# Optimization experiments

Hardware: AMD Instinct MI355X
Metric: run time of the kernel (lower is better)

The kernel has to match this reference:

```python
import jax, jax.numpy as jnp
import numpy as np

C_M, C_Z, NO_BINS = 256, 128, 15
MIN_BIN, MAX_BIN, INF = 3.25, 20.75, 1e8
LN_EPS = 1e-5


def _layer_norm(t, w, b):
    mu = jnp.mean(t, axis=-1, keepdims=True)
    var = jnp.var(t, axis=-1, keepdims=True)
    return (t - mu) * jax.lax.rsqrt(var + LN_EPS) * w + b


def setup_inputs() -> dict:
    key = jax.random.key(0)
    ks = jax.random.split(key, 8)
    B, N = 1, 768
    m = jax.random.normal(ks[0], (B, N, C_M), dtype=jnp.float32)
    z = jax.random.normal(ks[1], (B, N, N, C_Z), dtype=jnp.float32)
    # scale coords so pairwise distances span the 3.25-20.75 A bin range
    x = jax.random.normal(ks[2], (B, N, 3), dtype=jnp.float32) * 10.0
    seqs = jax.random.normal(ks[3], (B, N, 21), dtype=jnp.float32)
    lin_w = jax.random.normal(ks[4], (C_Z, NO_BINS), dtype=jnp.float32) * 0.1
    lin_b = jnp.zeros((C_Z,), dtype=jnp.float32)
    ln_m_w = jnp.ones((C_M,), dtype=jnp.float32)
    ln_m_b = jnp.zeros((C_M,), dtype=jnp.float32)
    ln_z_w = jnp.ones((C_Z,), dtype=jnp.float32)
    ln_z_b = jnp.zeros((C_Z,), dtype=jnp.float32)
    return {"m": m, "z": z, "x": x, "seqs": seqs,
            "lin_w": lin_w, "lin_b": lin_b,
            "ln_m_w": ln_m_w, "ln_m_b": ln_m_b,
            "ln_z_w": ln_z_w, "ln_z_b": ln_z_b}


def reference(m, z, x, seqs, lin_w, lin_b, ln_m_w, ln_m_b, ln_z_w, ln_z_b):
    # m update: LayerNorm only (track_seq_states=False, seqs unused)
    m_update = _layer_norm(m, ln_m_w, ln_m_b)

    bins = jnp.linspace(MIN_BIN, MAX_BIN, NO_BINS, dtype=x.dtype)
    sq_bins = bins ** 2
    upper = jnp.concatenate([sq_bins[1:], jnp.array([INF], dtype=x.dtype)])

    # pairwise squared distances [*, N, N, 1]
    diff = x[..., :, None, :] - x[..., None, :, :]
    d = jnp.sum(diff ** 2, axis=-1, keepdims=True)
    # one-hot distogram [*, N, N, no_bins] (strict inequalities, matching torch)
    oh = ((d > sq_bins) & (d < upper)).astype(x.dtype)
    # Linear(no_bins -> c_z)
    d_emb = jnp.einsum('...b,cb->...c', oh, lin_w) + lin_b

    z_update = d_emb + _layer_norm(z, ln_z_w, ln_z_b)
    return (m_update, z_update)
```

## Files before the change

kernel.cpp:

```cpp
#include <hip/hip_runtime.h>

#define LN_EPS 1e-5f
#define C_M 256
#define C_Z 128
#define NO_BINS 15

typedef float f4 __attribute__((ext_vector_type(4)));

__device__ __forceinline__ f4 f4zero() { f4 t = {0.f, 0.f, 0.f, 0.f}; return t; }

__device__ __forceinline__ int bin_of_xj(const float* __restrict__ x,
                                         const float* sqb, int i,
                                         float xj0, float xj1, float xj2)
{
    const float dx = x[3 * i + 0] - xj0;
    const float dy = x[3 * i + 1] - xj1;
    const float dz = x[3 * i + 2] - xj2;
    const float d = __fadd_rn(__fadd_rn(__fmul_rn(dx, dx), __fmul_rn(dy, dy)),
                              __fmul_rn(dz, dz));
    int cnt = 0;
#pragma unroll
    for (int k = 0; k < NO_BINS; ++k) {
        const float bk = 3.25f + 1.25f * (float)k;
        cnt += (d > bk * bk) ? 1 : 0;
    }
    return ((cnt > 0) && (d < 1e8f) && (d != sqb[cnt])) ? cnt - 1 : -1;
}

__device__ __forceinline__ void ln_stats(const f4 v, float& s, float& s2)
{
    s  = v.x + v.y + v.z + v.w;
    s2 = v.x * v.x + v.y * v.y + v.z * v.z + v.w * v.w;
}

__global__ __launch_bounds__(256, 6) void fused_uniform(
    const float* __restrict__ m, const float* __restrict__ ln_m_w,
    const float* __restrict__ ln_m_b, float* __restrict__ out_m, int m_rows,
    const float* __restrict__ z, const float* __restrict__ x,
    const float* __restrict__ lin_w, const float* __restrict__ lin_b,
    const float* __restrict__ ln_z_w, const float* __restrict__ ln_z_b,
    float* __restrict__ out_z, int N, int iters)
{
    __shared__ float lw[NO_BINS * C_Z];
    __shared__ float sqb[16];
    const int tid = threadIdx.x;
    for (int t = tid; t < NO_BINS * C_Z; t += 256) {
        const int c = t / NO_BINS;
        const int bin = t - c * NO_BINS;
        lw[bin * C_Z + c] = lin_w[t];
    }
    if (tid < 16) {
        const float bk = 3.25f + 1.25f * (float)tid;
        sqb[tid] = (tid < NO_BINS) ? bk * bk : -1.0f;
    }
    __syncthreads();

    if ((int)blockIdx.x < ((m_rows + 3) >> 2)) {
        const int wid    = tid >> 6;
        const int lane64 = tid & 63;
        const int row    = blockIdx.x * 4 + wid;
        if (row < m_rows) {
            const f4 v = reinterpret_cast<const f4*>(m + (long long)row * C_M)[lane64];
            float s, s2; ln_stats(v, s, s2);
#pragma unroll
            for (int msk = 1; msk < 64; msk <<= 1) {
                s  += __shfl_xor(s,  msk);
                s2 += __shfl_xor(s2, msk);
            }
            const float mu  = s * (1.0f / C_M);
            const float inv = rsqrtf(s2 * (1.0f / C_M) - mu * mu + LN_EPS);
            const f4 wv = reinterpret_cast<const f4*>(ln_m_w)[lane64];
            const f4 bv = reinterpret_cast<const f4*>(ln_m_b)[lane64];
            f4 o = (v - mu) * inv * wv + bv;
            reinterpret_cast<f4*>(out_m + (long long)row * C_M)[lane64] = o;
        }
    }

    const int half = tid >> 5;
    const int lane = tid & 31;

    const f4 wv = reinterpret_cast<const f4*>(ln_z_w)[lane];
    f4 bv = reinterpret_cast<const f4*>(ln_z_b)[lane];
    bv += reinterpret_cast<const f4*>(lin_b)[lane];

    const int slot = (int)blockIdx.x * 8 + half;
    const long long stride = (long long)N * 16;
    int i = slot / N;
    const int j = slot - i * N;

    const float xj0 = x[3 * j + 0];
    const float xj1 = x[3 * j + 1];
    const float xj2 = x[3 * j + 2];

    long long r = slot;
    for (int t = 0; t < iters; t += 4) {
        const long long r0 = r, r1 = r + stride, r2 = r + 2 * stride, r3 = r + 3 * stride;
        const int i0 = i, i1 = i + 16, i2 = i + 32, i3 = i + 48;

        const f4 v0 = reinterpret_cast<const f4*>(z + r0 * C_Z)[lane];
        const f4 v1 = reinterpret_cast<const f4*>(z + r1 * C_Z)[lane];
        const f4 v2 = reinterpret_cast<const f4*>(z + r2 * C_Z)[lane];
        const f4 v3 = reinterpret_cast<const f4*>(z + r3 * C_Z)[lane];

        const int b0 = bin_of_xj(x, sqb, i0, xj0, xj1, xj2);
        const int b1 = bin_of_xj(x, sqb, i1, xj0, xj1, xj2);
        const int b2 = bin_of_xj(x, sqb, i2, xj0, xj1, xj2);
        const int b3 = bin_of_xj(x, sqb, i3, xj0, xj1, xj2);

        f4 e0 = f4zero(), e1 = f4zero(), e2 = f4zero(), e3 = f4zero();
        if (b0 >= 0) e0 = reinterpret_cast<const f4*>(lw + b0 * C_Z)[lane];
        if (b1 >= 0) e1 = reinterpret_cast<const f4*>(lw + b1 * C_Z)[lane];
        if (b2 >= 0) e2 = reinterpret_cast<const f4*>(lw + b2 * C_Z)[lane];
        if (b3 >= 0) e3 = reinterpret_cast<const f4*>(lw + b3 * C_Z)[lane];

        float s0, q0, s1, q1, s2, q2, s3, q3;
        ln_stats(v0, s0, q0); ln_stats(v1, s1, q1);
        ln_stats(v2, s2, q2); ln_stats(v3, s3, q3);
#pragma unroll
        for (int msk = 1; msk < 32; msk <<= 1) {
            s0 += __shfl_xor(s0, msk); q0 += __shfl_xor(q0, msk);
            s1 += __shfl_xor(s1, msk); q1 += __shfl_xor(q1, msk);
            s2 += __shfl_xor(s2, msk); q2 += __shfl_xor(q2, msk);
            s3 += __shfl_xor(s3, msk); q3 += __shfl_xor(q3, msk);
        }
        const float mu0 = s0 * (1.0f / C_Z), iv0 = rsqrtf(q0 * (1.0f / C_Z) - mu0 * mu0 + LN_EPS);
        const float mu1 = s1 * (1.0f / C_Z), iv1 = rsqrtf(q1 * (1.0f / C_Z) - mu1 * mu1 + LN_EPS);
        const float mu2 = s2 * (1.0f / C_Z), iv2 = rsqrtf(q2 * (1.0f / C_Z) - mu2 * mu2 + LN_EPS);
        const float mu3 = s3 * (1.0f / C_Z), iv3 = rsqrtf(q3 * (1.0f / C_Z) - mu3 * mu3 + LN_EPS);

        f4 o0 = (v0 - mu0) * iv0 * wv + bv + e0;
        f4 o1 = (v1 - mu1) * iv1 * wv + bv + e1;
        f4 o2 = (v2 - mu2) * iv2 * wv + bv + e2;
        f4 o3 = (v3 - mu3) * iv3 * wv + bv + e3;
        __builtin_nontemporal_store(o0, reinterpret_cast<f4*>(out_z + r0 * C_Z) + lane);
        __builtin_nontemporal_store(o1, reinterpret_cast<f4*>(out_z + r1 * C_Z) + lane);
        __builtin_nontemporal_store(o2, reinterpret_cast<f4*>(out_z + r2 * C_Z) + lane);
        __builtin_nontemporal_store(o3, reinterpret_cast<f4*>(out_z + r3 * C_Z) + lane);

        r += 4 * stride;
        i += 64;
    }
}

__device__ __forceinline__ int bin_of(const float* __restrict__ x,
                                      const float* sqb, int i, int j)
{
    return bin_of_xj(x, sqb, i, x[3 * j], x[3 * j + 1], x[3 * j + 2]);
}

__global__ __launch_bounds__(256) void fused_generic(
    const float* __restrict__ m, const float* __restrict__ ln_m_w,
    const float* __restrict__ ln_m_b, float* __restrict__ out_m, int m_rows,
    const float* __restrict__ z, const float* __restrict__ x,
    const float* __restrict__ lin_w, const float* __restrict__ lin_b,
    const float* __restrict__ ln_z_w, const float* __restrict__ ln_z_b,
    float* __restrict__ out_z, int N)
{
    __shared__ float lw[NO_BINS * C_Z];
    __shared__ float sqb[16];
    const int tid = threadIdx.x;
    for (int t = tid; t < NO_BINS * C_Z; t += 256) {
        const int c = t / NO_BINS;
        const int bin = t - c * NO_BINS;
        lw[bin * C_Z + c] = lin_w[t];
    }
    if (tid < 16) {
        const float bk = 3.25f + 1.25f * (float)tid;
        sqb[tid] = (tid < NO_BINS) ? bk * bk : -1.0f;
    }
    __syncthreads();

    if ((int)blockIdx.x < ((m_rows + 3) >> 2)) {
        const int wid    = tid >> 6;
        const int lane64 = tid & 63;
        const int row    = blockIdx.x * 4 + wid;
        if (row < m_rows) {
            const f4 v = reinterpret_cast<const f4*>(m + (long long)row * C_M)[lane64];
            float s, s2; ln_stats(v, s, s2);
#pragma unroll
            for (int msk = 1; msk < 64; msk <<= 1) {
                s  += __shfl_xor(s,  msk);
                s2 += __shfl_xor(s2, msk);
            }
            const float mu  = s * (1.0f / C_M);
            const float inv = rsqrtf(s2 * (1.0f / C_M) - mu * mu + LN_EPS);
            const f4 wv = reinterpret_cast<const f4*>(ln_m_w)[lane64];
            const f4 bv = reinterpret_cast<const f4*>(ln_m_b)[lane64];
            f4 o = (v - mu) * inv * wv + bv;
            reinterpret_cast<f4*>(out_m + (long long)row * C_M)[lane64] = o;
        }
    }

    const int half = tid >> 5;
    const int lane = tid & 31;
    const f4 wv = reinterpret_cast<const f4*>(ln_z_w)[lane];
    f4 bv = reinterpret_cast<const f4*>(ln_z_b)[lane];
    bv += reinterpret_cast<const f4*>(lin_b)[lane];

    const long long total  = (long long)N * N;
    const long long stride = (long long)gridDim.x * 8;
    for (long long r = (long long)blockIdx.x * 8 + half; r < total; r += stride) {
        const int i = (int)(r / N);
        const int j = (int)(r - (long long)i * N);
        const f4 v = reinterpret_cast<const f4*>(z + r * C_Z)[lane];
        const int bin = bin_of(x, sqb, i, j);
        f4 e = f4zero();
        if (bin >= 0) e = reinterpret_cast<const f4*>(lw + bin * C_Z)[lane];
        float s, s2; ln_stats(v, s, s2);
#pragma unroll
        for (int msk = 1; msk < 32; msk <<= 1) {
            s  += __shfl_xor(s,  msk);
            s2 += __shfl_xor(s2, msk);
        }
        const float mu  = s * (1.0f / C_Z);
        const float inv = rsqrtf(s2 * (1.0f / C_Z) - mu * mu + LN_EPS);
        f4 o = (v - mu) * inv * wv + bv + e;
        __builtin_nontemporal_store(o, reinterpret_cast<f4*>(out_z + r * C_Z) + lane);
    }
}

extern "C" void kernel_launch(void* const* d_in, const int* in_sizes, int n_in,
                              void* d_out, int out_size, void* d_ws, size_t ws_size,
                              hipStream_t stream) {
    const float* m      = (const float*)d_in[0];
    const float* z      = (const float*)d_in[1];
    const float* x      = (const float*)d_in[2];
    const float* lin_w  = (const float*)d_in[4];
    const float* lin_b  = (const float*)d_in[5];
    const float* ln_m_w = (const float*)d_in[6];
    const float* ln_m_b = (const float*)d_in[7];
    const float* ln_z_w = (const float*)d_in[8];
    const float* ln_z_b = (const float*)d_in[9];

    const int N = in_sizes[0] / C_M;
    float* out_m = (float*)d_out;
    float* out_z = out_m + (long long)N * C_M;

    if ((N % 16) == 0 && 2 * N >= (N + 3) / 4) {
        fused_uniform<<<2 * N, 256, 0, stream>>>(m, ln_m_w, ln_m_b, out_m, N,
                                                 z, x, lin_w, lin_b, ln_z_w, ln_z_b,
                                                 out_z, N, N / 16);
    } else {
        int g = 2048;
        const int mB = (N + 3) / 4;
        if (g < mB) g = mB;
        fused_generic<<<g, 256, 0, stream>>>(m, ln_m_w, ln_m_b, out_m, N,
                                             z, x, lin_w, lin_b, ln_z_w, ln_z_b,
                                             out_z, N);
    }
}
```

Baseline: 109.9 us.

## Use fixed 2048-block grid-stride schedule with higher occupancy bound

```diff
diff --git a/kernel.cpp b/kernel.cpp
--- a/kernel.cpp
+++ b/kernel.cpp
@@ -9,13 +9,12 @@
 
 __device__ __forceinline__ f4 f4zero() { f4 t = {0.f, 0.f, 0.f, 0.f}; return t; }
 
-__device__ __forceinline__ int bin_of_xj(const float* __restrict__ x,
-                                         const float* sqb, int i,
-                                         float xj0, float xj1, float xj2)
-{
-    const float dx = x[3 * i + 0] - xj0;
-    const float dy = x[3 * i + 1] - xj1;
-    const float dz = x[3 * i + 2] - xj2;
+__device__ __forceinline__ int bin_of(const float* __restrict__ x,
+                                      const float* sqb, int i, int j)
+{
+    const float dx = x[3 * i + 0] - x[3 * j + 0];
+    const float dy = x[3 * i + 1] - x[3 * j + 1];
+    const float dz = x[3 * i + 2] - x[3 * j + 2];
     const float d = __fadd_rn(__fadd_rn(__fmul_rn(dx, dx), __fmul_rn(dy, dy)),
                               __fmul_rn(dz, dz));
     int cnt = 0;
@@ -33,13 +32,13 @@
     s2 = v.x * v.x + v.y * v.y + v.z * v.z + v.w * v.w;
 }
 
-__global__ __launch_bounds__(256, 6) void fused_uniform(
+__global__ __launch_bounds__(256, 8) void fused_occ(
     const float* __restrict__ m, const float* __restrict__ ln_m_w,
     const float* __restrict__ ln_m_b, float* __restrict__ out_m, int m_rows,
     const float* __restrict__ z, const float* __restrict__ x,
     const float* __restrict__ lin_w, const float* __restrict__ lin_b,
     const float* __restrict__ ln_z_w, const float* __restrict__ ln_z_b,
-    float* __restrict__ out_z, int N, int iters)
+    float* __restrict__ out_z, int N, int phases, int di, int rem)
 {
     __shared__ float lw[NO_BINS * C_Z];
     __shared__ float sqb[16];
@@ -84,28 +83,29 @@
     bv += reinterpret_cast<const f4*>(lin_b)[lane];
 
     const int slot = (int)blockIdx.x * 8 + half;
-    const long long stride = (long long)N * 16;
+    const long long S = (long long)gridDim.x * 8;
     int i = slot / N;
-    const int j = slot - i * N;
-
-    const float xj0 = x[3 * j + 0];
-    const float xj1 = x[3 * j + 1];
-    const float xj2 = x[3 * j + 2];
+    int j = slot - i * N;
 
     long long r = slot;
-    for (int t = 0; t < iters; t += 4) {
-        const long long r0 = r, r1 = r + stride, r2 = r + 2 * stride, r3 = r + 3 * stride;
-        const int i0 = i, i1 = i + 16, i2 = i + 32, i3 = i + 48;
+    for (int p = 0; p < phases; p += 4) {
+        const int i0 = i, j0 = j;
+        int i1 = i0 + di, j1 = j0 + rem; if (j1 >= N) { j1 -= N; ++i1; }
+        int i2 = i1 + di, j2 = j1 + rem; if (j2 >= N) { j2 -= N; ++i2; }
+        int i3 = i2 + di, j3 = j2 + rem; if (j3 >= N) { j3 -= N; ++i3; }
+        i = i3 + di; j = j3 + rem; if (j >= N) { j -= N; ++i; }
+
+        const long long r0 = r, r1 = r + S, r2 = r + 2 * S, r3 = r + 3 * S;
 
         const f4 v0 = reinterpret_cast<const f4*>(z + r0 * C_Z)[lane];
         const f4 v1 = reinterpret_cast<const f4*>(z + r1 * C_Z)[lane];
         const f4 v2 = reinterpret_cast<const f4*>(z + r2 * C_Z)[lane];
         const f4 v3 = reinterpret_cast<const f4*>(z + r3 * C_Z)[lane];
 
-        const int b0 = bin_of_xj(x, sqb, i0, xj0, xj1, xj2);
-        const int b1 = bin_of_xj(x, sqb, i1, xj0, xj1, xj2);
-        const int b2 = bin_of_xj(x, sqb, i2, xj0, xj1, xj2);
-        const int b3 = bin_of_xj(x, sqb, i3, xj0, xj1, xj2);
+        const int b0 = bin_of(x, sqb, i0, j0);
+        const int b1 = bin_of(x, sqb, i1, j1);
+        const int b2 = bin_of(x, sqb, i2, j2);
+        const int b3 = bin_of(x, sqb, i3, j3);
 
         f4 e0 = f4zero(), e1 = f4zero(), e2 = f4zero(), e3 = f4zero();
         if (b0 >= 0) e0 = reinterpret_cast<const f4*>(lw + b0 * C_Z)[lane];
@@ -137,15 +137,8 @@
         __builtin_nontemporal_store(o2, reinterpret_cast<f4*>(out_z + r2 * C_Z) + lane);
         __builtin_nontemporal_store(o3, reinterpret_cast<f4*>(out_z + r3 * C_Z) + lane);
 
-        r += 4 * stride;
-        i += 64;
-    }
-}
-
-__device__ __forceinline__ int bin_of(const float* __restrict__ x,
-                                      const float* sqb, int i, int j)
-{
-    return bin_of_xj(x, sqb, i, x[3 * j], x[3 * j + 1], x[3 * j + 2]);
+        r += 4 * S;
+    }
 }
 
 __global__ __launch_bounds__(256) void fused_generic(
@@ -236,13 +229,20 @@
     float* out_m = (float*)d_out;
     float* out_z = out_m + (long long)N * C_M;
 
-    if ((N % 16) == 0 && 2 * N >= (N + 3) / 4) {
-        fused_uniform<<<2 * N, 256, 0, stream>>>(m, ln_m_w, ln_m_b, out_m, N,
-                                                 z, x, lin_w, lin_b, ln_z_w, ln_z_b,
-                                                 out_z, N, N / 16);
+    const long long total = (long long)N * N;
+    const int G = 2048;
+    const long long S = (long long)G * 8;
+    const int mB = (N + 3) / 4;
+
+    if (total % S == 0 && (total / S) % 4 == 0 && G >= mB) {
+        const int phases = (int)(total / S);
+        const int di  = (int)(S / N);
+        const int rem = (int)(S % N);
+        fused_occ<<<G, 256, 0, stream>>>(m, ln_m_w, ln_m_b, out_m, N,
+                                         z, x, lin_w, lin_b, ln_z_w, ln_z_b,
+                                         out_z, N, phases, di, rem);
     } else {
         int g = 2048;
-        const int mB = (N + 3) / 4;
         if (g < mB) g = mB;
         fused_generic<<<g, 256, 0, stream>>>(m, ln_m_w, ln_m_b, out_m, N,
                                              z, x, lin_w, lin_b, ln_z_w, ln_z_b,
```

After: 149.9 us. 36.3% more time.
